# Kernel optimization log

Measured on AMD Instinct MI355X. Metric: run time of the kernel, lower is better.

Reference implementation:

```python
import jax, jax.numpy as jnp
import numpy as np

B = 16384
DIM_IN = 128; DIM_OUT = 128; DIM_X = 512; DIM_NL = 128
EPS = 1e-3; ALPHA = 1.0; STD = 0.5
DIM_H = 2 * DIM_X + DIM_NL


def setup_inputs() -> dict:
    key = jax.random.key(0)
    ks = jax.random.split(key, 8)
    u_in = jax.random.normal(ks[0], (B, 1, DIM_IN), jnp.float32)
    X = STD * jax.random.normal(ks[1], (DIM_H, DIM_H), jnp.float32)
    Y = STD * jax.random.normal(ks[2], (DIM_X, DIM_X), jnp.float32)
    B2 = STD * jax.random.normal(ks[3], (DIM_X, DIM_IN), jnp.float32)
    C2 = STD * jax.random.normal(ks[4], (DIM_OUT, DIM_X), jnp.float32)
    D21 = STD * jax.random.normal(ks[5], (DIM_OUT, DIM_NL), jnp.float32)
    D22 = STD * jax.random.normal(ks[6], (DIM_OUT, DIM_IN), jnp.float32)
    D12 = STD * jax.random.normal(ks[7], (DIM_NL, DIM_IN), jnp.float32)
    x0 = jnp.zeros((1, 1, DIM_X), jnp.float32)
    return {"u_in": u_in, "X": X, "Y": Y, "B2": B2, "C2": C2,
            "D21": D21, "D22": D22, "D12": D12, "x0": x0}


def reference(u_in, X, Y, B2, C2, D21, D22, D12, x0):
    # --- derived contractive parameterization (torch _update_model_param) ---
    H = X.T @ X + EPS * jnp.eye(DIM_H, dtype=X.dtype)
    H11 = H[:DIM_X, :DIM_X]
    H21 = H[DIM_X:DIM_X + DIM_NL, :DIM_X]
    H22 = H[DIM_X:DIM_X + DIM_NL, DIM_X:DIM_X + DIM_NL]
    H31 = H[DIM_X + DIM_NL:, :DIM_X]
    H32 = H[DIM_X + DIM_NL:, DIM_X:DIM_X + DIM_NL]
    H33 = H[DIM_X + DIM_NL:, DIM_X + DIM_NL:]
    F = H31                               # [X, X]
    B1 = H32                              # [X, NL]
    E = 0.5 * (H11 + ALPHA * H33 + Y - Y.T)  # [X, X]
    Lam = 0.5 * jnp.diagonal(H22)            # [NL]
    D11 = -jnp.tril(H22, k=-1)               # strictly lower triangular [NL, NL]
    C1 = -H21                                # [NL, X]

    u = u_in[:, 0, :]      # [B, in]
    x = x0[0, 0, :]        # [X], broadcast over batch as in torch
    xc = C1 @ x            # [NL] (x @ C1row^T per row, shared across batch)
    ud = u @ D12.T         # [B, NL] (precomputed; same math as per-row matmul)

    # sequential forward-substitution with tanh per row (strict lower tri D11)
    def step(w, inp):
        i, d11row, xci, lam = inp
        v = xci + ud[:, i] + w @ d11row        # [B]
        return w.at[:, i].set(jnp.tanh(v / lam)), None

    w0 = jnp.zeros((u.shape[0], DIM_NL), u.dtype)
    w, _ = jax.lax.scan(step, w0, (jnp.arange(DIM_NL), D11, xc, Lam))

    # state update: x+ = (x F^T + w B1^T + u B2^T) E^{-T}
    pre = (F @ x)[None, :] + w @ B1.T + u @ B2.T   # [B, X]
    x_new = pre @ jnp.linalg.inv(E).T              # [B, X]
    # output
    y = x_new @ C2.T + w @ D21.T + u @ D22.T       # [B, out]
    return y[:, None, :]
```

## Files before the change

kernel.cpp:

```cpp
#include <hip/hip_runtime.h>
#include <math.h>

#define EPS_C 0.001f
#define BATCH 16384

__global__ __launch_bounds__(256) void k_xtx(const float* __restrict__ X, float* __restrict__ H) {
  __shared__ float smem[64 * 65];
  const int bi64 = blockIdx.x, bj64 = blockIdx.y;
  if (bi64 > bj64) return;
  float (*sA)[65] = (float(*)[65])smem;
  float (*sB)[65] = (float(*)[65])(smem + 32 * 65);
  const int t = threadIdx.x;
  const int bi = bi64 * 64, bj = bj64 * 64;
  const int tj = t & 15, ti = t >> 4;
  float acc[4][4] = {};
  for (int k0 = 0; k0 < 1152; k0 += 32) {
    #pragma unroll
    for (int l = 0; l < 2; ++l) {
      int idx = t + l * 256;
      int kk = idx >> 4, c4 = (idx & 15) << 2;
      float4 va = *(const float4*)&X[(k0 + kk) * 1152 + bi + c4];
      sA[kk][c4 + 0] = va.x; sA[kk][c4 + 1] = va.y; sA[kk][c4 + 2] = va.z; sA[kk][c4 + 3] = va.w;
      float4 vb = *(const float4*)&X[(k0 + kk) * 1152 + bj + c4];
      sB[kk][c4 + 0] = vb.x; sB[kk][c4 + 1] = vb.y; sB[kk][c4 + 2] = vb.z; sB[kk][c4 + 3] = vb.w;
    }
    __syncthreads();
    #pragma unroll
    for (int kk = 0; kk < 32; ++kk) {
      float am[4], bn[4];
      #pragma unroll
      for (int q = 0; q < 4; ++q) am[q] = sA[kk][ti * 4 + q];
      #pragma unroll
      for (int q = 0; q < 4; ++q) bn[q] = sB[kk][tj * 4 + q];
      #pragma unroll
      for (int r = 0; r < 4; ++r)
        #pragma unroll
        for (int c = 0; c < 4; ++c)
          acc[r][c] = fmaf(am[r], bn[c], acc[r][c]);
    }
    __syncthreads();
  }
  #pragma unroll
  for (int r = 0; r < 4; ++r) {
    int gi = bi + ti * 4 + r;
    float vv[4];
    #pragma unroll
    for (int c = 0; c < 4; ++c) {
      vv[c] = acc[r][c];
      if (gi == bj + tj * 4 + c) vv[c] += EPS_C;
    }
    float4 o = make_float4(vv[0], vv[1], vv[2], vv[3]);
    *(float4*)&H[gi * 1152 + bj + tj * 4] = o;
  }
  if (bi64 < bj64) {
    float (*tr)[65] = (float(*)[65])smem;
    #pragma unroll
    for (int r = 0; r < 4; ++r)
      #pragma unroll
      for (int c = 0; c < 4; ++c)
        tr[tj * 4 + c][ti * 4 + r] = acc[r][c];
    __syncthreads();
    #pragma unroll
    for (int l = 0; l < 4; ++l) {
      int e = t + l * 256;
      int row = e >> 4, c4 = (e & 15) << 2;
      float4 o = make_float4(tr[row][c4], tr[row][c4 + 1], tr[row][c4 + 2], tr[row][c4 + 3]);
      *(float4*)&H[(bj + row) * 1152 + bi + c4] = o;
    }
  }
}

__global__ __launch_bounds__(256) void k_assemble(const float* __restrict__ H, const float* __restrict__ Y,
                           const float* __restrict__ C2, const float* __restrict__ x0,
                           float* __restrict__ M, float* __restrict__ D11,
                           float* __restrict__ Lam, float* __restrict__ xc, float* __restrict__ Fx) {
  const int b = blockIdx.x;
  const int t = threadIdx.x;
  if (b < 256) {
    __shared__ float tA[32][33], tB[32][33], tC[32][33];
    const int R0 = (b & 15) * 32, C0 = (b >> 4) * 32;
    const int c = t & 31, rr = t >> 5;
    #pragma unroll
    for (int p = 0; p < 4; ++p) {
      int row = rr + p * 8;
      tA[row][c] = H[(C0 + row) * 1152 + R0 + c];
      tB[row][c] = H[(640 + C0 + row) * 1152 + 640 + R0 + c];
      tC[row][c] = Y[(C0 + row) * 512 + R0 + c];
    }
    __syncthreads();
    #pragma unroll
    for (int p = 0; p < 4; ++p) {
      int r = rr + p * 8;
      float val = 0.5f * (tA[c][r] + tB[c][r] + tC[c][r] - Y[(R0 + r) * 512 + C0 + c]);
      M[(R0 + r) * 640 + C0 + c] = val;
    }
  } else if (b < 320) {
    int e0 = (b - 256) * 1024;
    #pragma unroll
    for (int l = 0; l < 4; ++l) {
      int e = e0 + l * 256 + t;
      int r = e >> 7, o = e & 127;
      M[r * 640 + 512 + o] = C2[o * 512 + r];
    }
  } else if (b < 384) {
    int e = (b - 320) * 256 + t;
    int i = e >> 7, j = e & 127;
    D11[e] = (j < i) ? -H[(512 + i) * 1152 + 512 + j] : 0.0f;
  } else if (b == 384) {
    if (t < 128) Lam[t] = 0.5f * H[(512 + t) * 1152 + 512 + t];
  } else if (b == 385) {
    if (t < 128) {
      float s = 0.f;
      for (int a = 0; a < 512; ++a) s = fmaf(H[(512 + t) * 1152 + a], x0[a], s);
      xc[t] = -s;
    }
  } else {
    int r = (b - 386) * 256 + t;
    float s = 0.f;
    for (int a = 0; a < 512; ++a) s = fmaf(H[(640 + r) * 1152 + a], x0[a], s);
    Fx[r] = s;
  }
}

__global__ __launch_bounds__(64) void k_lu_dp(float* __restrict__ M, float* __restrict__ Dfac, int kb) {
  __shared__ float sD[64 * 65];
  __shared__ float sRD[64];
  const int t = threadIdx.x;
  const int nU = 9 - kb;
  const int pb = blockIdx.x;
  float v[64];
  int c = 0, rr = 0;
  if (pb < nU) {
    c = 64 * (kb + 1) + pb * 64 + t;
    #pragma unroll
    for (int i = 0; i < 64; ++i) v[i] = M[(kb * 64 + i) * 640 + c];
  } else {
    rr = 64 * (kb + 1) + (pb - nU) * 64 + t;
    #pragma unroll
    for (int i = 0; i < 16; ++i) *(float4*)&v[i * 4] = *(const float4*)&M[rr * 640 + kb * 64 + i * 4];
  }
  {
    const float* blk = M + kb * 64 * 640 + kb * 64;
    float col[64];
    #pragma unroll
    for (int r = 0; r < 64; ++r) col[r] = blk[r * 640 + t];
    float invp = 1.0f;
    #pragma unroll
    for (int k = 0; k < 64; ++k) {
      float piv = __shfl(col[k], k);
      float inv = 1.0f / piv;
      if (t == k) invp = inv;
      float m = col[k] * inv;
      bool act = t > k;
      #pragma unroll
      for (int r = k + 1; r < 64; ++r) {
        float ckr = __shfl(col[r], k);
        if (act) col[r] -= ckr * m;
      }
    }
    #pragma unroll
    for (int r = 0; r < 64; ++r) {
      if (r > t) col[r] *= invp;
      sD[r * 65 + t] = col[r];
      if (pb == 0) Dfac[kb * 4096 + r * 64 + t] = col[r];
    }
    sRD[t] = invp;
  }
  __syncthreads();
  if (pb < nU) {
    #pragma unroll
    for (int i = 1; i < 64; ++i) {
      float a0 = v[i], a1 = 0.f;
      #pragma unroll
      for (int j = 0; j < i; j += 2) {
        a0 = fmaf(-sD[i * 65 + j], v[j], a0);
        if (j + 1 < i) a1 = fmaf(-sD[i * 65 + j + 1], v[j + 1], a1);
      }
      v[i] = a0 + a1;
    }
    #pragma unroll
    for (int i = 0; i < 64; ++i) M[(kb * 64 + i) * 640 + c] = v[i];
  } else {
    #pragma unroll
    for (int j = 0; j < 64; ++j) {
      float a0 = v[j], a1 = 0.f;
      #pragma unroll
      for (int i = 0; i < j; i += 2) {
        a0 = fmaf(-v[i], sD[i * 65 + j], a0);
        if (i + 1 < j) a1 = fmaf(-v[i + 1], sD[(i + 1) * 65 + j], a1);
      }
      v[j] = (a0 + a1) * sRD[j];
    }
    #pragma unroll
    for (int i = 0; i < 16; ++i) *(float4*)&M[rr * 640 + kb * 64 + i * 4] = *(float4*)&v[i * 4];
  }
}

__global__ __launch_bounds__(256) void k_lu_trailing(float* __restrict__ M, int kb) {
  __shared__ float sL[32][65];
  __shared__ float sU[32][65];
  const int t = threadIdx.x;
  const int base = 64 * (kb + 1);
  const int r0 = base + blockIdx.y * 64, c0 = base + blockIdx.x * 64;
  const int tj = t & 15, ti = t >> 4;
  float acc[4][4] = {};
  for (int k0 = 0; k0 < 64; k0 += 32) {
    #pragma unroll
    for (int l = 0; l < 2; ++l) {
      int idx = t + l * 256;
      int row = idx >> 3, k4 = (idx & 7) << 2;
      float4 v = *(const float4*)&M[(r0 + row) * 640 + kb * 64 + k0 + k4];
      sL[k4 + 0][row] = v.x; sL[k4 + 1][row] = v.y; sL[k4 + 2][row] = v.z; sL[k4 + 3][row] = v.w;
      int kk = idx >> 4, c4 = (idx & 15) << 2;
      float4 u4 = *(const float4*)&M[(kb * 64 + k0 + kk) * 640 + c0 + c4];
      sU[kk][c4 + 0] = u4.x; sU[kk][c4 + 1] = u4.y; sU[kk][c4 + 2] = u4.z; sU[kk][c4 + 3] = u4.w;
    }
    __syncthreads();
    #pragma unroll
    for (int kk = 0; kk < 32; ++kk) {
      float am[4], bn[4];
      #pragma unroll
      for (int q = 0; q < 4; ++q) am[q] = sL[kk][ti * 4 + q];
      #pragma unroll
      for (int q = 0; q < 4; ++q) bn[q] = sU[kk][tj * 4 + q];
      #pragma unroll
      for (int r = 0; r < 4; ++r)
        #pragma unroll
        for (int c = 0; c < 4; ++c)
          acc[r][c] = fmaf(am[r], bn[c], acc[r][c]);
    }
    __syncthreads();
  }
  #pragma unroll
  for (int r = 0; r < 4; ++r) {
    float4 old = *(float4*)&M[(r0 + ti * 4 + r) * 640 + c0 + tj * 4];
    old.x -= acc[r][0]; old.y -= acc[r][1]; old.z -= acc[r][2]; old.w -= acc[r][3];
    *(float4*)&M[(r0 + ti * 4 + r) * 640 + c0 + tj * 4] = old;
  }
}

__global__ __launch_bounds__(64) void k_inv(const float* __restrict__ Dfac, float* __restrict__ invU) {
  __shared__ float sD[64 * 65];
  __shared__ float srs[64];
  const int t = threadIdx.x;
  const int kb = blockIdx.x;
  for (int l = 0; l < 64; ++l) sD[l * 65 + t] = Dfac[kb * 4096 + l * 64 + t];
  __syncthreads();
  srs[t] = 1.0f / sD[t * 65 + t];
  __syncthreads();
  float v[64];
  #pragma unroll
  for (int i = 0; i < 64; ++i) v[i] = (i == t) ? srs[t] : 0.0f;
  #pragma unroll
  for (int i = 62; i >= 0; --i) {
    float a0 = 0.f, a1 = 0.f;
    #pragma unroll
    for (int j = i + 1; j < 64; j += 2) {
      a0 = fmaf(-sD[i * 65 + j], v[j], a0);
      if (j + 1 < 64) a1 = fmaf(-sD[i * 65 + j + 1], v[j + 1], a1);
    }
    float nv = (a0 + a1) * srs[i];
    v[i] = (i == t) ? v[i] : nv;
  }
  #pragma unroll
  for (int i = 0; i < 64; ++i) invU[kb * 4096 + i * 64 + t] = v[i];
}

__global__ __launch_bounds__(512, 2) void k_bs(const float* __restrict__ M, const float* __restrict__ invUg,
                                               float* __restrict__ Gt) {
  __shared__ float sZ[512 * 17];
  __shared__ float sU[64 * 65];
  __shared__ float sI[64 * 65];
  const int t = threadIdx.x;
  const int c0 = blockIdx.x * 16;
  const int o = t & 15, q = t >> 4;
  #pragma unroll
  for (int l = 0; l < 16; ++l) {
    int e = t + l * 512;
    int r = e >> 4, oo = e & 15;
    sZ[r * 17 + oo] = M[r * 640 + 512 + c0 + oo];
  }
  for (int kb = 7; kb >= 0; --kb) {
    #pragma unroll
    for (int l = 0; l < 8; ++l) {
      int e = t + l * 512;
      int r = e >> 6, k = e & 63;
      sI[r * 65 + k] = invUg[kb * 4096 + r * 64 + k];
    }
    __syncthreads();
    float xv[2];
    #pragma unroll
    for (int rr = 0; rr < 2; ++rr) {
      int i = q * 2 + rr;
      float a0 = 0.f, a1 = 0.f;
      #pragma unroll
      for (int k = 0; k < 64; k += 2) {
        a0 = fmaf(sI[i * 65 + k], sZ[(kb * 64 + k) * 17 + o], a0);
        a1 = fmaf(sI[i * 65 + k + 1], sZ[(kb * 64 + k + 1) * 17 + o], a1);
      }
      xv[rr] = a0 + a1;
    }
    __syncthreads();
    #pragma unroll
    for (int rr = 0; rr < 2; ++rr) {
      int i = q * 2 + rr;
      sZ[(kb * 64 + i) * 17 + o] = xv[rr];
      Gt[(kb * 64 + i) * 128 + c0 + o] = xv[rr];
    }
    __syncthreads();
    if (kb == 0) break;
    float xk[64];
    #pragma unroll
    for (int k = 0; k < 64; ++k) xk[k] = sZ[(kb * 64 + k) * 17 + o];
    float bufA[8], bufB[8];
    #pragma unroll
    for (int l = 0; l < 8; ++l) {
      int e = t + l * 512;
      int r = e >> 6, k = e & 63;
      bufA[l] = M[r * 640 + kb * 64 + k];
    }
    for (int i = 0; i < kb; ++i) {
      #pragma unroll
      for (int l = 0; l < 8; ++l) {
        int e = t + l * 512;
        int r = e >> 6, k = e & 63;
        sU[r * 65 + k] = bufA[l];
      }
      if (i + 1 < kb) {
        #pragma unroll
        for (int l = 0; l < 8; ++l) {
          int e = t + l * 512;
          int r = e >> 6, k = e & 63;
          bufB[l] = M[((i + 1) * 64 + r) * 640 + kb * 64 + k];
        }
      }
      __syncthreads();
      #pragma unroll
      for (int rr = 0; rr < 2; ++rr) {
        int row = q * 2 + rr;
        float acc = sZ[(i * 64 + row) * 17 + o];
        #pragma unroll
        for (int k = 0; k < 64; ++k)
          acc = fmaf(-sU[row * 65 + k], xk[k], acc);
        sZ[(i * 64 + row) * 17 + o] = acc;
      }
      #pragma unroll
      for (int l = 0; l < 8; ++l) bufA[l] = bufB[l];
      __syncthreads();
    }
  }
}

__global__ void k_wass(const float* __restrict__ Gt, const float* __restrict__ H,
                       const float* __restrict__ B2, const float* __restrict__ D21,
                       const float* __restrict__ D22, const float* __restrict__ Fx,
                       float* __restrict__ W1, float* __restrict__ W2, float* __restrict__ bias) {
  int idx = blockIdx.x * 256 + threadIdx.x;
  if (idx < 16384) {
    int o = idx >> 7, j = idx & 127;
    float s = 0.f;
    for (int a = 0; a < 512; ++a) s = fmaf(Gt[a * 128 + o], H[(640 + a) * 1152 + 512 + j], s);
    W1[idx] = s + D21[idx];
  } else if (idx < 32768) {
    int q = idx - 16384;
    int o = q >> 7, j = q & 127;
    float s = 0.f;
    for (int a = 0; a < 512; ++a) s = fmaf(Gt[a * 128 + o], B2[a * 128 + j], s);
    W2[q] = s + D22[q];
  } else if (idx < 32768 + 128) {
    int o = idx - 32768;
    float s = 0.f;
    for (int a = 0; a < 512; ++a) s = fmaf(Gt[a * 128 + o], Fx[a], s);
    bias[o] = s;
  }
}

__global__ __launch_bounds__(256) void k_ud(const float* __restrict__ u, const float* __restrict__ D12,
                                            const float* __restrict__ xc, float* __restrict__ baseT) {
  __shared__ float sU[32][65];
  __shared__ float sD[32][65];
  const int t = threadIdx.x;
  const int b0 = blockIdx.x * 64, i0 = blockIdx.y * 64;
  const int tm = t & 15, tn = t >> 4;
  float acc[4][4] = {};
  for (int k0 = 0; k0 < 128; k0 += 32) {
    #pragma unroll
    for (int l = 0; l < 2; ++l) {
      int idx = t + l * 256;
      int row = idx >> 3, k4 = (idx & 7) << 2;
      float4 v = *(const float4*)&u[(b0 + row) * 128 + k0 + k4];
      sU[k4 + 0][row] = v.x; sU[k4 + 1][row] = v.y; sU[k4 + 2][row] = v.z; sU[k4 + 3][row] = v.w;
      float4 d = *(const float4*)&D12[(i0 + row) * 128 + k0 + k4];
      sD[k4 + 0][row] = d.x; sD[k4 + 1][row] = d.y; sD[k4 + 2][row] = d.z; sD[k4 + 3][row] = d.w;
    }
    __syncthreads();
    #pragma unroll
    for (int kk = 0; kk < 32; ++kk) {
      float mm[4], nn[4];
      #pragma unroll
      for (int q = 0; q < 4; ++q) mm[q] = sU[kk][tm * 4 + q];
      #pragma unroll
      for (int q = 0; q < 4; ++q) nn[q] = sD[kk][tn * 4 + q];
      #pragma unroll
      for (int c = 0; c < 4; ++c)
        #pragma unroll
        for (int r = 0; r < 4; ++r)
          acc[c][r] = fmaf(nn[c], mm[r], acc[c][r]);
    }
    __syncthreads();
  }
  #pragma unroll
  for (int c = 0; c < 4; ++c) {
    int i = i0 + tn * 4 + c;
    float xcv = xc[i];
    float4 v = make_float4(acc[c][0] + xcv, acc[c][1] + xcv, acc[c][2] + xcv, acc[c][3] + xcv);
    *(float4*)&baseT[i * BATCH + b0 + tm * 4] = v;
  }
}

__global__ __launch_bounds__(64, 1) void k_scan(const float* __restrict__ baseT, const float* __restrict__ D11g,
                                                const float* __restrict__ Lam, float* __restrict__ wT) {
  __shared__ float wl[32 * 260];
  const int t = threadIdx.x;
  const int b = blockIdx.x * 64 + t;
  for (int c = 0; c < 8; ++c) {
    const int C = c * 16;
    float bt[16];
    #pragma unroll
    for (int l = 0; l < 16; ++l) bt[l] = baseT[(C + l) * BATCH + b];
    float hist[16];
    #pragma unroll
    for (int l = 0; l < 16; ++l) hist[l] = 0.f;
    for (int g = 0; g < C / 4; ++g) {
      float4 wv = *(const float4*)&wl[g * 260 + t * 4];
      #pragma unroll
      for (int li = 0; li < 16; ++li) {
        const float* __restrict__ Dr = D11g + (C + li) * 128 + g * 4;
        float h = hist[li];
        h = fmaf(wv.x, Dr[0], h);
        h = fmaf(wv.y, Dr[1], h);
        h = fmaf(wv.z, Dr[2], h);
        h = fmaf(wv.w, Dr[3], h);
        hist[li] = h;
      }
    }
    float wc[16];
    #pragma unroll
    for (int li = 0; li < 16; ++li) {
      const int i = C + li;
      const float* __restrict__ Drow = D11g + i * 128;
      float a0 = bt[li], a1 = hist[li], a2 = 0.f, a3 = 0.f;
      #pragma unroll
      for (int lg = 0; lg + 4 <= li; lg += 4) {
        a0 = fmaf(wc[lg + 0], Drow[C + lg + 0], a0);
        a1 = fmaf(wc[lg + 1], Drow[C + lg + 1], a1);
        a2 = fmaf(wc[lg + 2], Drow[C + lg + 2], a2);
        a3 = fmaf(wc[lg + 3], Drow[C + lg + 3], a3);
      }
      #pragma unroll
      for (int lj = li & ~3; lj < li; ++lj) a0 = fmaf(wc[lj], Drow[C + lj], a0);
      float zv = ((a0 + a1) + (a2 + a3)) / Lam[i];
      float az = fabsf(zv);
      float e = __expf(-2.0f * az);
      float th = (1.0f - e) / (1.0f + e);
      wc[li] = copysignf(th, zv);
    }
    #pragma unroll
    for (int gg = 0; gg < 4; ++gg) {
      float4 o = make_float4(wc[gg * 4 + 0], wc[gg * 4 + 1], wc[gg * 4 + 2], wc[gg * 4 + 3]);
      *(float4*)&wl[(C / 4 + gg) * 260 + t * 4] = o;
    }
    #pragma unroll
    for (int li = 0; li < 16; ++li) wT[(C + li) * BATCH + b] = wc[li];
  }
}

__global__ __launch_bounds__(256) void k_y(const float* __restrict__ wT, const float* __restrict__ u,
                                           const float* __restrict__ W1, const float* __restrict__ W2,
                                           const float* __restrict__ bias, float* __restrict__ y) {
  __shared__ float sA[32][65];
  __shared__ float sW[32][65];
  const int t = threadIdx.x;
  const int b0 = blockIdx.x * 64, o0 = blockIdx.y * 64;
  const int tn = t & 15, tm = t >> 4;
  float acc[4][4] = {};
  for (int k0 = 0; k0 < 128; k0 += 32) {
    #pragma unroll
    for (int l = 0; l < 2; ++l) {
      int idx = t + l * 256;
      int kk = idx >> 4, c4 = (idx & 15) << 2;
      float4 v = *(const float4*)&wT[(k0 + kk) * BATCH + b0 + c4];
      sA[kk][c4 + 0] = v.x; sA[kk][c4 + 1] = v.y; sA[kk][c4 + 2] = v.z; sA[kk][c4 + 3] = v.w;
      int row = idx >> 3, k4 = (idx & 7) << 2;
      float4 d = *(const float4*)&W1[(o0 + row) * 128 + k0 + k4];
      sW[k4 + 0][row] = d.x; sW[k4 + 1][row] = d.y; sW[k4 + 2][row] = d.z; sW[k4 + 3][row] = d.w;
    }
    __syncthreads();
    #pragma unroll
    for (int kk = 0; kk < 32; ++kk) {
      float mm[4], nn[4];
      #pragma unroll
      for (int q = 0; q < 4; ++q) mm[q] = sA[kk][tm * 4 + q];
      #pragma unroll
      for (int q = 0; q < 4; ++q) nn[q] = sW[kk][tn * 4 + q];
      #pragma unroll
      for (int r = 0; r < 4; ++r)
        #pragma unroll
        for (int c = 0; c < 4; ++c)
          acc[r][c] = fmaf(mm[r], nn[c], acc[r][c]);
    }
    __syncthreads();
  }
  for (int k0 = 0; k0 < 128; k0 += 32) {
    #pragma unroll
    for (int l = 0; l < 2; ++l) {
      int idx = t + l * 256;
      int row = idx >> 3, k4 = (idx & 7) << 2;
      float4 v = *(const float4*)&u[(b0 + row) * 128 + k0 + k4];
      sA[k4 + 0][row] = v.x; sA[k4 + 1][row] = v.y; sA[k4 + 2][row] = v.z; sA[k4 + 3][row] = v.w;
      float4 d = *(const float4*)&W2[(o0 + row) * 128 + k0 + k4];
      sW[k4 + 0][row] = d.x; sW[k4 + 1][row] = d.y; sW[k4 + 2][row] = d.z; sW[k4 + 3][row] = d.w;
    }
    __syncthreads();
    #pragma unroll
    for (int kk = 0; kk < 32; ++kk) {
      float mm[4], nn[4];
      #pragma unroll
      for (int q = 0; q < 4; ++q) mm[q] = sA[kk][tm * 4 + q];
      #pragma unroll
      for (int q = 0; q < 4; ++q) nn[q] = sW[kk][tn * 4 + q];
      #pragma unroll
      for (int r = 0; r < 4; ++r)
        #pragma unroll
        for (int c = 0; c < 4; ++c)
          acc[r][c] = fmaf(mm[r], nn[c], acc[r][c]);
    }
    __syncthreads();
  }
  #pragma unroll
  for (int r = 0; r < 4; ++r) {
    int bb = b0 + tm * 4 + r;
    float4 v = make_float4(acc[r][0] + bias[o0 + tn * 4 + 0],
                           acc[r][1] + bias[o0 + tn * 4 + 1],
                           acc[r][2] + bias[o0 + tn * 4 + 2],
                           acc[r][3] + bias[o0 + tn * 4 + 3]);
    *(float4*)&y[bb * 128 + o0 + tn * 4] = v;
  }
}

extern "C" void kernel_launch(void* const* d_in, const int* in_sizes, int n_in,
                              void* d_out, int out_size, void* d_ws, size_t ws_size,
                              hipStream_t stream) {
  const float* u   = (const float*)d_in[0];
  const float* X   = (const float*)d_in[1];
  const float* Y   = (const float*)d_in[2];
  const float* B2  = (const float*)d_in[3];
  const float* C2  = (const float*)d_in[4];
  const float* D21 = (const float*)d_in[5];
  const float* D22 = (const float*)d_in[6];
  const float* D12 = (const float*)d_in[7];
  const float* x0  = (const float*)d_in[8];

  float* ws = (float*)d_ws;
  float* H     = ws;
  float* M     = H + 1327104;
  float* Gt    = M + 327680;
  float* W1    = Gt + 65536;
  float* W2    = W1 + 16384;
  float* D11   = W2 + 16384;
  float* Lam   = D11 + 16384;
  float* xc    = Lam + 128;
  float* Fx    = xc + 128;
  float* bias  = Fx + 512;
  float* baseT = bias + 128 + 64;
  float* wT    = baseT;
  float* Dfac  = H;
  float* invUg = H + 32768;
  float* y     = (float*)d_out;

  k_xtx<<<dim3(18, 18), 256, 0, stream>>>(X, H);
  k_assemble<<<388, 256, 0, stream>>>(H, Y, C2, x0, M, D11, Lam, xc, Fx);

  for (int kb = 0; kb < 8; ++kb) {
    k_lu_dp<<<16 - 2 * kb, 64, 0, stream>>>(M, Dfac, kb);
    if (kb < 7)
      k_lu_trailing<<<dim3(9 - kb, 7 - kb), 256, 0, stream>>>(M, kb);
  }

  k_inv<<<8, 64, 0, stream>>>(Dfac, invUg);
  k_bs<<<8, 512, 0, stream>>>(M, invUg, Gt);
  k_wass<<<129, 256, 0, stream>>>(Gt, H, B2, D21, D22, Fx, W1, W2, bias);

  k_ud<<<dim3(256, 2), 256, 0, stream>>>(u, D12, xc, baseT);
  k_scan<<<256, 64, 0, stream>>>(baseT, D11, Lam, wT);
  k_y<<<dim3(256, 2), 256, 0, stream>>>(wT, u, W1, W2, bias, y);
}
```

Measured before the change: 902.4 us.

## Split scan history accumulation across four wavefronts per block

The scan kernel goes from one wavefront to four per block. Each wavefront computes the history dot products for 4 of the 16 rows in the current chunk and shares them through shared memory. Wavefront 0 then runs the sequential in-chunk forward substitution with tanh. The aim is to spread the O(C) history work, which dominates later chunks, across more lanes and raise occupancy on the 256-block grid, at the cost of two block barriers per chunk and three wavefronts sitting idle during the serial part.

```diff
diff --git a/kernel.cpp b/kernel.cpp
--- a/kernel.cpp
+++ b/kernel.cpp
@@ -418,60 +418,68 @@
   }
 }
 
-__global__ __launch_bounds__(64, 1) void k_scan(const float* __restrict__ baseT, const float* __restrict__ D11g,
-                                                const float* __restrict__ Lam, float* __restrict__ wT) {
+__global__ __launch_bounds__(256, 1) void k_scan(const float* __restrict__ baseT, const float* __restrict__ D11g,
+                                                 const float* __restrict__ Lam, float* __restrict__ wT) {
   __shared__ float wl[32 * 260];
-  const int t = threadIdx.x;
+  __shared__ float hl[16 * 68];
+  const int t = threadIdx.x & 63;
+  const int w = threadIdx.x >> 6;
   const int b = blockIdx.x * 64 + t;
   for (int c = 0; c < 8; ++c) {
     const int C = c * 16;
     float bt[16];
-    #pragma unroll
-    for (int l = 0; l < 16; ++l) bt[l] = baseT[(C + l) * BATCH + b];
-    float hist[16];
-    #pragma unroll
-    for (int l = 0; l < 16; ++l) hist[l] = 0.f;
+    if (w == 0) {
+      #pragma unroll
+      for (int l = 0; l < 16; ++l) bt[l] = baseT[(C + l) * BATCH + b];
+    }
+    float h0 = 0.f, h1 = 0.f, h2 = 0.f, h3 = 0.f;
     for (int g = 0; g < C / 4; ++g) {
       float4 wv = *(const float4*)&wl[g * 260 + t * 4];
+      const float* __restrict__ D0 = D11g + (C + w * 4 + 0) * 128 + g * 4;
+      const float* __restrict__ D1 = D11g + (C + w * 4 + 1) * 128 + g * 4;
+      const float* __restrict__ D2 = D11g + (C + w * 4 + 2) * 128 + g * 4;
+      const float* __restrict__ D3 = D11g + (C + w * 4 + 3) * 128 + g * 4;
+      h0 = fmaf(wv.x, D0[0], h0); h0 = fmaf(wv.y, D0[1], h0); h0 = fmaf(wv.z, D0[2], h0); h0 = fmaf(wv.w, D0[3], h0);
+      h1 = fmaf(wv.x, D1[0], h1); h1 = fmaf(wv.y, D1[1], h1); h1 = fmaf(wv.z, D1[2], h1); h1 = fmaf(wv.w, D1[3], h1);
+      h2 = fmaf(wv.x, D2[0], h2); h2 = fmaf(wv.y, D2[1], h2); h2 = fmaf(wv.z, D2[2], h2); h2 = fmaf(wv.w, D2[3], h2);
+      h3 = fmaf(wv.x, D3[0], h3); h3 = fmaf(wv.y, D3[1], h3); h3 = fmaf(wv.z, D3[2], h3); h3 = fmaf(wv.w, D3[3], h3);
+    }
+    hl[(w * 4 + 0) * 68 + t] = h0;
+    hl[(w * 4 + 1) * 68 + t] = h1;
+    hl[(w * 4 + 2) * 68 + t] = h2;
+    hl[(w * 4 + 3) * 68 + t] = h3;
+    __syncthreads();
+    if (w == 0) {
+      float wc[16];
       #pragma unroll
       for (int li = 0; li < 16; ++li) {
-        const float* __restrict__ Dr = D11g + (C + li) * 128 + g * 4;
-        float h = hist[li];
-        h = fmaf(wv.x, Dr[0], h);
-        h = fmaf(wv.y, Dr[1], h);
-        h = fmaf(wv.z, Dr[2], h);
-        h = fmaf(wv.w, Dr[3], h);
-        hist[li] = h;
-      }
-    }
-    float wc[16];
-    #pragma unroll
-    for (int li = 0; li < 16; ++li) {
-      const int i = C + li;
-      const float* __restrict__ Drow = D11g + i * 128;
-      float a0 = bt[li], a1 = hist[li], a2 = 0.f, a3 = 0.f;
-      #pragma unroll
-      for (int lg = 0; lg + 4 <= li; lg += 4) {
-        a0 = fmaf(wc[lg + 0], Drow[C + lg + 0], a0);
-        a1 = fmaf(wc[lg + 1], Drow[C + lg + 1], a1);
-        a2 = fmaf(wc[lg + 2], Drow[C + lg + 2], a2);
-        a3 = fmaf(wc[lg + 3], Drow[C + lg + 3], a3);
-      }
-      #pragma unroll
-      for (int lj = li & ~3; lj < li; ++lj) a0 = fmaf(wc[lj], Drow[C + lj], a0);
-      float zv = ((a0 + a1) + (a2 + a3)) / Lam[i];
-      float az = fabsf(zv);
-      float e = __expf(-2.0f * az);
-      float th = (1.0f - e) / (1.0f + e);
-      wc[li] = copysignf(th, zv);
-    }
-    #pragma unroll
-    for (int gg = 0; gg < 4; ++gg) {
-      float4 o = make_float4(wc[gg * 4 + 0], wc[gg * 4 + 1], wc[gg * 4 + 2], wc[gg * 4 + 3]);
-      *(float4*)&wl[(C / 4 + gg) * 260 + t * 4] = o;
-    }
-    #pragma unroll
-    for (int li = 0; li < 16; ++li) wT[(C + li) * BATCH + b] = wc[li];
+        const int i = C + li;
+        const float* __restrict__ Drow = D11g + i * 128;
+        float a0 = bt[li], a1 = hl[li * 68 + t], a2 = 0.f, a3 = 0.f;
+        #pragma unroll
+        for (int lg = 0; lg + 4 <= li; lg += 4) {
+          a0 = fmaf(wc[lg + 0], Drow[C + lg + 0], a0);
+          a1 = fmaf(wc[lg + 1], Drow[C + lg + 1], a1);
+          a2 = fmaf(wc[lg + 2], Drow[C + lg + 2], a2);
+          a3 = fmaf(wc[lg + 3], Drow[C + lg + 3], a3);
+        }
+        #pragma unroll
+        for (int lj = li & ~3; lj < li; ++lj) a0 = fmaf(wc[lj], Drow[C + lj], a0);
+        float zv = ((a0 + a1) + (a2 + a3)) / Lam[i];
+        float az = fabsf(zv);
+        float e = __expf(-2.0f * az);
+        float th = (1.0f - e) / (1.0f + e);
+        wc[li] = copysignf(th, zv);
+      }
+      #pragma unroll
+      for (int gg = 0; gg < 4; ++gg) {
+        float4 o = make_float4(wc[gg * 4 + 0], wc[gg * 4 + 1], wc[gg * 4 + 2], wc[gg * 4 + 3]);
+        *(float4*)&wl[(C / 4 + gg) * 260 + t * 4] = o;
+      }
+      #pragma unroll
+      for (int li = 0; li < 16; ++li) wT[(C + li) * BATCH + b] = wc[li];
+    }
+    __syncthreads();
   }
 }
 
@@ -592,6 +600,6 @@
   k_wass<<<129, 256, 0, stream>>>(Gt, H, B2, D21, D22, Fx, W1, W2, bias);
 
   k_ud<<<dim3(256, 2), 256, 0, stream>>>(u, D12, xc, baseT);
-  k_scan<<<256, 64, 0, stream>>>(baseT, D11, Lam, wT);
+  k_scan<<<256, 256, 0, stream>>>(baseT, D11, Lam, wT);
   k_y<<<dim3(256, 2), 256, 0, stream>>>(wT, u, W1, W2, bias, y);
 }
```

New measurement: 846.5 us. 1.07x faster.
